# Optimization experiments

Hardware: AMD Instinct MI355X
Metric: run time of the kernel (lower is better)

Reference implementation:

```python
import jax, jax.numpy as jnp
import numpy as np
from jax.scipy.special import i0

# torchkbnufft default configuration
N = 256          # image size per dim (im_size)
OSF = 2          # grid oversampling factor (default grid_size = 2*im_size)
G = N * OSF      # oversampled grid size = 512
W = 6            # kernel width (numpoints default)
ALPHA = 2.34 * W # Kaiser-Bessel shape parameter (kbwidth default 2.34)
M = 65536        # number of non-uniform k-space samples
B, C = 2, 8      # batch, coils


def _kb_ft(t):
    """Analytic Fourier transform of the KB kernel (for deapodization)."""
    s2 = ALPHA ** 2 - (jnp.pi * W * t) ** 2
    z = jnp.sqrt(jnp.abs(s2)) + 1e-12
    return jnp.where(s2 >= 0, jnp.sinh(z) / z, jnp.sin(z) / z)


def _kb(d):
    """Kaiser-Bessel interpolation kernel, d = distance in grid units."""
    u = 1.0 - (2.0 * d / W) ** 2
    return jnp.where(u > 0, i0(ALPHA * jnp.sqrt(jnp.maximum(u, 1e-12))), 0.0) / W


def setup_inputs() -> dict:
    key = jax.random.key(0)
    k1, k2 = jax.random.split(key)
    x_image = jax.random.normal(k1, (B, C, N, N), dtype=jnp.float32)
    # trajectory in radians/sample, uniform in [-pi, pi)
    k_traj = (jax.random.uniform(k2, (2, M), dtype=jnp.float32) - 0.5) * (2 * jnp.pi)
    return {"x_image": x_image, "k_traj": k_traj}


def reference(x_image, k_traj):
    # 1) deapodization (scaling coefficients), centered image convention
    n = jnp.arange(N, dtype=jnp.float32) - N / 2
    sc = 1.0 / _kb_ft(n / G)                       # (N,)
    xs = (x_image * (sc[:, None] * sc[None, :])).astype(jnp.complex64)

    # 2) zero-pad onto oversampled grid with image centered at index 0 (mod G)
    grid = jnp.zeros(x_image.shape[:2] + (G, G), jnp.complex64)
    grid = grid.at[..., :N, :N].set(xs)
    grid = jnp.roll(grid, shift=(-(N // 2), -(N // 2)), axis=(-2, -1))
    Xk = jnp.fft.fft2(grid)                        # (B,C,G,G) uniform k-space

    # 3) KB interpolation onto non-uniform points (irregular gather)
    tm = k_traj * (G / (2 * jnp.pi))               # continuous grid coords, (2,M)
    offs = jnp.arange(-(W // 2) + 1, W // 2 + 1, dtype=jnp.float32)  # [-2..3]
    base = jnp.floor(tm)
    pts = base[:, :, None] + offs                  # (2,M,W) neighbor coords
    wts = _kb(tm[:, :, None] - pts)                # (2,M,W) real weights
    idx = pts.astype(jnp.int32) % G                # wrap (periodic grid)

    gathered = Xk[:, :, idx[0][:, :, None], idx[1][:, None, :]]  # (B,C,M,W,W)
    y = jnp.einsum('bcmij,mi,mj->bcm', gathered,
                   wts[0].astype(jnp.complex64), wts[1].astype(jnp.complex64))
    # return complex result as stacked (real, imag) float32 for the harness
    return jnp.stack([y.real, y.imag], axis=-1)   # (B,C,M,2)
```

## Files before the change

kernel.cpp:

```cpp
#include <hip/hip_runtime.h>
#include <hip/hip_fp16.h>
#include <math.h>

#define NN 256
#define GSZ 512
#define GG (GSZ * GSZ)
#define BC 16
#define MM 65536
#define ALPHA_C 14.04f
#define WKER 6
#define PI_F 3.14159265358979f
#define RC2 0.70710678118654752f
#define KSCALE 81.48733086305042f

#define SSCALE 16777216.0f
#define INV_SSCALE 5.9604644775390625e-8f

#define CAP 160
#define TRW 21
#define TPITCH 23
#define PLANE (TRW * TPITCH)
#define NPT16 (BC * TRW * TRW)

__device__ __forceinline__ __half2* gh_plane(float2* grid, int bc) {
    return (__half2*)((char*)grid + (size_t)bc * (GG * 8) + 524288);
}
__device__ __forceinline__ const __half2* gh_plane_c(const float2* grid, int bc) {
    return (const __half2*)((const char*)grid + (size_t)bc * (GG * 8) + 524288);
}


__device__ __forceinline__ float bessel_i0(float x) {
    if (x < 3.75f) {
        float t = x * (1.0f / 3.75f);
        float t2 = t * t;
        return 1.0f + t2 * (3.5156229f + t2 * (3.0899424f + t2 * (1.2067492f +
                     t2 * (0.2659732f + t2 * (0.0360768f + t2 * 0.0045813f)))));
    } else {
        float t = 3.75f / x;
        float p = 0.39894228f + t * (0.01328592f + t * (0.00225319f + t * (-0.00157565f +
                  t * (0.00916281f + t * (-0.02057706f + t * (0.02635537f +
                  t * (-0.01647633f + t * 0.00392377f)))))));
        return p * __expf(x) * rsqrtf(x);
    }
}

__device__ __forceinline__ float kb_weight(float d) {
    float r = d * (2.0f / (float)WKER);
    float u = 1.0f - r * r;
    if (u <= 0.0f) return 0.0f;
    return bessel_i0(ALPHA_C * sqrtf(u)) * (1.0f / (float)WKER);
}

__device__ __forceinline__ float kb_ft_inv(float t) {
    float a = PI_F * (float)WKER * t;
    float s2 = ALPHA_C * ALPHA_C - a * a;
    float z = sqrtf(fabsf(s2)) + 1e-12f;
    float sh = 0.5f * (__expf(z) - __expf(-z));
    return z / sh;
}

__device__ __forceinline__ void cmul(float& zr, float& zi, float wr, float wi) {
    float r = zr * wr - zi * wi;
    zi = zr * wi + zi * wr;
    zr = r;
}


template <int L>
__device__ __forceinline__ void radix8_stage(float* pr, float* pi_, int j) {
    int pos = j & (L - 1);
    int base = (j - pos) * 8 + pos;
    float ar[8], ai[8];
#pragma unroll
    for (int r = 0; r < 8; ++r) {
        int idx = base + r * L;
        int ph = idx + (idx >> 3);
        ar[r] = pr[ph];
        ai[r] = pi_[ph];
    }
    if (L > 1) {
        float th = (float)pos * (-PI_F / (4.0f * (float)L));
        float s1, c1;
        __sincosf(th, &s1, &c1);
        float wr = c1, wi = s1;
#pragma unroll
        for (int r = 1; r < 8; ++r) {
            cmul(ar[r], ai[r], wr, wi);
            float nr = wr * c1 - wi * s1;
            wi = wr * s1 + wi * c1;
            wr = nr;
        }
    }
    float s0r = ar[0] + ar[4], s0i = ai[0] + ai[4];
    float d0r = ar[0] - ar[4], d0i = ai[0] - ai[4];
    float s1r = ar[2] + ar[6], s1i = ai[2] + ai[6];
    float d1r = ar[2] - ar[6], d1i = ai[2] - ai[6];
    float E0r = s0r + s1r, E0i = s0i + s1i;
    float E2r = s0r - s1r, E2i = s0i - s1i;
    float E1r = d0r + d1i, E1i = d0i - d1r;
    float E3r = d0r - d1i, E3i = d0i + d1r;
    float u0r = ar[1] + ar[5], u0i = ai[1] + ai[5];
    float v0r = ar[1] - ar[5], v0i = ai[1] - ai[5];
    float u1r = ar[3] + ar[7], u1i = ai[3] + ai[7];
    float v1r = ar[3] - ar[7], v1i = ai[3] - ai[7];
    float O0r = u0r + u1r, O0i = u0i + u1i;
    float O2r = u0r - u1r, O2i = u0i - u1i;
    float O1r = v0r + v1i, O1i = v0i - v1r;
    float O3r = v0r - v1i, O3i = v0i + v1r;
    float t1r = RC2 * (O1r + O1i), t1i = RC2 * (O1i - O1r);
    float t2r = O2i,               t2i = -O2r;
    float t3r = RC2 * (O3i - O3r), t3i = -RC2 * (O3r + O3i);
    float xr[8], xi[8];
    xr[0] = E0r + O0r; xi[0] = E0i + O0i;
    xr[4] = E0r - O0r; xi[4] = E0i - O0i;
    xr[1] = E1r + t1r; xi[1] = E1i + t1i;
    xr[5] = E1r - t1r; xi[5] = E1i - t1i;
    xr[2] = E2r + t2r; xi[2] = E2i + t2i;
    xr[6] = E2r - t2r; xi[6] = E2i - t2i;
    xr[3] = E3r + t3r; xi[3] = E3i + t3i;
    xr[7] = E3r - t3r; xi[7] = E3i - t3i;
#pragma unroll
    for (int q = 0; q < 8; ++q) {
        int idx = base + q * L;
        int ph = idx + (idx >> 3);
        pr[ph] = xr[q];
        pi_[ph] = xi[q];
    }
}


#define LDSP 576
__global__ void __launch_bounds__(256) k_fft_row(const float* __restrict__ x,
                                                 float2* __restrict__ grid) {
    __shared__ float re[4][LDSP], im[4][LDSP];
    int b = blockIdx.x;
    int t = threadIdx.x;
    int w = t >> 6;
    int l = t & 63;
    int rg = (b & 63) * 4 + w;
    int bc = b >> 6;
    int r = (rg < 128) ? rg : rg + 256;
    int r_img = rg ^ 128;
    float scx = kb_ft_inv((float)(r_img - 128) * (1.0f / (float)GSZ));
    const float* xrow = x + ((size_t)bc * NN + (size_t)r_img) * NN;
#pragma unroll
    for (int e = 0; e < 8; ++e) {
        int i = e * 64 + l;
        float v = 0.0f;
        if (i < 128 || i >= 384) {
            int y = (i + 128) & (GSZ - 1);
            float scy = kb_ft_inv((float)(y - 128) * (1.0f / (float)GSZ));
            v = xrow[y] * scx * scy;
        }
        int rev = (l & 7) * 64 + (l >> 3) * 8 + e;
        int ph = rev + (rev >> 3);
        re[w][ph] = v;
        im[w][ph] = 0.0f;
    }
    __syncthreads();
    radix8_stage<1>(re[w], im[w], l);
    __syncthreads();
    radix8_stage<8>(re[w], im[w], l);
    __syncthreads();
    radix8_stage<64>(re[w], im[w], l);
    __syncthreads();
    size_t gbase = (size_t)bc * GG + (size_t)r * GSZ;
#pragma unroll
    for (int e = 0; e < 8; ++e) {
        int k = e * 64 + l;
        int ph = k + (k >> 3);
        grid[gbase + k] = make_float2(re[w][ph], im[w][ph]);
    }
}

#define CSTR 577
__global__ void __launch_bounds__(256) k_fft_col(float2* __restrict__ grid) {
    __shared__ float re[16][CSTR], im[16][CSTR];
    int b = blockIdx.x;
    int bc = b >> 5;
    int c0 = (b & 31) << 4;
    size_t base = (size_t)bc * GG + (size_t)c0;
    int t = threadIdx.x;
#pragma unroll
    for (int it = 0; it < 32; ++it) {
        int idx = it * 256 + t;
        int row = idx >> 4, col = idx & 15;
        float2 v = make_float2(0.0f, 0.0f);
        if (row < 128 || row >= 384)
            v = grid[base + (size_t)row * GSZ + col];
        int rev = (row & 7) * 64 + ((row >> 3) & 7) * 8 + (row >> 6);
        int ph = rev + (rev >> 3);
        re[col][ph] = v.x;
        im[col][ph] = v.y;
    }
    __syncthreads();
    int col = t & 15, jg = t >> 4;
#pragma unroll
    for (int k = 0; k < 4; ++k) radix8_stage<1>(re[col], im[col], jg + 16 * k);
    __syncthreads();
#pragma unroll
    for (int k = 0; k < 4; ++k) radix8_stage<8>(re[col], im[col], jg + 16 * k);
    __syncthreads();
#pragma unroll
    for (int k = 0; k < 4; ++k) radix8_stage<64>(re[col], im[col], jg + 16 * k);
    __syncthreads();
    __half2* ghp = gh_plane(grid, bc);
#pragma unroll
    for (int it = 0; it < 32; ++it) {
        int idx = it * 256 + t;
        int row = idx >> 4, c = idx & 15;
        int ph = row + (row >> 3);
        ghp[(size_t)row * GSZ + c0 + c] = __float22half2_rn(
            make_float2(re[c][ph] * SSCALE, im[c][ph] * SSCALE));
    }
}


__global__ void k_bin(const float* __restrict__ kt, unsigned* __restrict__ cnt,
                      unsigned short* __restrict__ ubuf) {
    int m = blockIdx.x * blockDim.x + threadIdx.x;
    float tmx = kt[m] * KSCALE;
    float tmy = kt[MM + m] * KSCALE;
    int ibx = (int)floorf(tmx) & (GSZ - 1);
    int iby = (int)floorf(tmy) & (GSZ - 1);
    int tile = ((ibx >> 4) << 5) | (iby >> 4);
    unsigned slot = atomicAdd(&cnt[tile], 1u);
    if (slot < CAP) ubuf[(size_t)tile * CAP + slot] = (unsigned short)m;
}


__device__ __forceinline__ void load_tile(const float2* __restrict__ grid, int tile,
                                          int t, __half2* buf) {
    int tx0 = (tile >> 5) << 4;
    int ty0 = (tile & 31) << 4;
#pragma unroll
    for (int k = 0; k < 28; ++k) {
        int idx = t + (k << 8);
        if (idx < NPT16) {
            int bcp = idx / (TRW * TRW);
            int rem = idx - bcp * (TRW * TRW);
            int r = rem / TRW;
            int c = rem - r * TRW;
            int row = (tx0 - 2 + r) & (GSZ - 1);
            int col = (ty0 - 2 + c) & (GSZ - 1);
            buf[k] = gh_plane_c(grid, bcp)[(size_t)row * GSZ + col];
        }
    }
}

__global__ void __launch_bounds__(256) k_gather_tile(
    const float2* __restrict__ grid, const float* __restrict__ kt,
    const unsigned* __restrict__ cnt, const unsigned short* __restrict__ ubuf,
    float2* __restrict__ out) {
    __shared__ __half2 ldsh[BC * PLANE];
    __shared__ float wts[CAP][13];
    __shared__ unsigned lxy[CAP];
    int bid = blockIdx.x;
    int b = ((bid & 7) << 6) | (bid >> 3);
    int t = threadIdx.x;
    __half2 buf[28];
    load_tile(grid, 2 * b, t, buf);
    for (int k2 = 0; k2 < 2; ++k2) {
        int tile = 2 * b + k2;
        int n = (int)cnt[tile];
        if (n > CAP) n = CAP;
        __syncthreads();
#pragma unroll
        for (int k = 0; k < 28; ++k) {
            int idx = t + (k << 8);
            if (idx < NPT16) {
                int bcp = idx / (TRW * TRW);
                int rem = idx - bcp * (TRW * TRW);
                int r = rem / TRW;
                int c = rem - r * TRW;
                ldsh[bcp * PLANE + r * TPITCH + c] = buf[k];
            }
        }
        if (t < n) {
            int m = (int)ubuf[(size_t)tile * CAP + t];
            float tmx = kt[m] * KSCALE;
            float tmy = kt[MM + m] * KSCALE;
            float bx = floorf(tmx), by = floorf(tmy);
#pragma unroll
            for (int o = 0; o < 6; ++o) {
                float offv = (float)(o - 2);
                wts[t][o]     = kb_weight(tmx - (bx + offv)) * INV_SSCALE;
                wts[t][6 + o] = kb_weight(tmy - (by + offv));
            }
            int lx = (int)bx & 15;
            int ly = (int)by & 15;
            lxy[t] = ((unsigned)m << 8) | (unsigned)(lx << 4) | (unsigned)ly;
        }
        __syncthreads();
        if (k2 == 0) load_tile(grid, 2 * b + 1, t, buf);
        int g = t >> 6;
        int base0 = (4 * g) * PLANE;
        for (int s = (t & 63); s < n; s += 64) {
            unsigned lc = lxy[s];
            int m = (int)(lc >> 8);
            int lx = (int)((lc >> 4) & 15u);
            int ly = (int)(lc & 15u);
            float w0v[6], w1v[6];
#pragma unroll
            for (int o = 0; o < 6; ++o) {
                w0v[o] = wts[s][o];
                w1v[o] = wts[s][6 + o];
            }
            int off0 = base0 + lx * TPITCH + ly;
            float ar[4] = {0.f, 0.f, 0.f, 0.f};
            float ai[4] = {0.f, 0.f, 0.f, 0.f};
#pragma unroll
            for (int ii = 0; ii < 6; ++ii) {
                float wi = w0v[ii];
                int rowoff = off0 + ii * TPITCH;
#pragma unroll
                for (int j = 0; j < 6; ++j) {
                    float wv = wi * w1v[j];
                    int o = rowoff + j;
#pragma unroll
                    for (int bq = 0; bq < 4; ++bq) {
                        float2 v = __half22float2(ldsh[o + bq * PLANE]);
                        ar[bq] = fmaf(wv, v.x, ar[bq]);
                        ai[bq] = fmaf(wv, v.y, ai[bq]);
                    }
                }
            }
#pragma unroll
            for (int bq = 0; bq < 4; ++bq)
                out[(size_t)(4 * g + bq) * MM + m] = make_float2(ar[bq], ai[bq]);
        }
    }
}

__global__ void k_gather(const float2* __restrict__ grid, const float* __restrict__ kt,
                         float2* __restrict__ out) {
    int tid = blockIdx.x * blockDim.x + threadIdx.x;
    int m = tid & (MM - 1);
    int bc = tid >> 16;
    float tmx = kt[m] * KSCALE;
    float tmy = kt[MM + m] * KSCALE;
    float bx = floorf(tmx), by = floorf(tmy);
    int ibx = (int)bx, iby = (int)by;
    float w0[6], w1[6];
    int ix[6], iy[6];
#pragma unroll
    for (int o = 0; o < 6; ++o) {
        float offv = (float)(o - 2);
        w0[o] = kb_weight(tmx - (bx + offv)) * INV_SSCALE;
        w1[o] = kb_weight(tmy - (by + offv));
        ix[o] = (ibx + (o - 2) + GSZ) & (GSZ - 1);
        iy[o] = (iby + (o - 2) + GSZ) & (GSZ - 1);
    }
    const __half2* img = gh_plane_c(grid, bc);
    float ar = 0.0f, ai = 0.0f;
#pragma unroll
    for (int i = 0; i < 6; ++i) {
        const __half2* rowp = img + (size_t)ix[i] * GSZ;
        float wi = w0[i];
#pragma unroll
        for (int j = 0; j < 6; ++j) {
            float2 v = __half22float2(rowp[iy[j]]);
            float wv = wi * w1[j];
            ar = fmaf(wv, v.x, ar);
            ai = fmaf(wv, v.y, ai);
        }
    }
    out[(size_t)bc * MM + m] = make_float2(ar, ai);
}


extern "C" void kernel_launch(void* const* d_in, const int* in_sizes, int n_in,
                              void* d_out, int out_size, void* d_ws, size_t ws_size,
                              hipStream_t stream) {
    const float* x = (const float*)d_in[0];
    const float* kt = (const float*)d_in[1];
    float2* out = (float2*)d_out;
    char* ws = (char*)d_ws;

    const size_t GRID_BYTES = (size_t)BC * GG * sizeof(float2);
    const size_t CNT_BYTES = 1024 * sizeof(unsigned);
    const size_t UBUF_BYTES = (size_t)1024 * CAP * sizeof(unsigned short);
    float2* grid = (float2*)ws;
    unsigned* cnt = (unsigned*)(ws + GRID_BYTES);
    unsigned short* ubuf = (unsigned short*)(ws + GRID_BYTES + CNT_BYTES);
    const size_t NEED = GRID_BYTES + CNT_BYTES + UBUF_BYTES;

    if (ws_size >= NEED) {
        hipMemsetAsync(cnt, 0, CNT_BYTES, stream);
        k_bin<<<MM / 256, 256, 0, stream>>>(kt, cnt, ubuf);
        k_fft_row<<<BC * 64, 256, 0, stream>>>(x, grid);
        k_fft_col<<<BC * (GSZ / 16), 256, 0, stream>>>(grid);
        k_gather_tile<<<512, 256, 0, stream>>>(grid, kt, cnt, ubuf, out);
    } else {
        k_fft_row<<<BC * 64, 256, 0, stream>>>(x, grid);
        k_fft_col<<<BC * (GSZ / 16), 256, 0, stream>>>(grid);
        k_gather<<<(BC * MM) / 256, 256, 0, stream>>>(grid, kt, out);
    }
}
```

Baseline: 76.07 us.

## Split gather tile work across coil quads with smaller blocks

After: 77.50 us. Within noise of the previous version (+1.9%).

```diff
diff --git a/kernel.cpp b/kernel.cpp
--- a/kernel.cpp
+++ b/kernel.cpp
@@ -20,7 +20,8 @@
 #define TRW 21
 #define TPITCH 23
 #define PLANE (TRW * TPITCH)
-#define NPT16 (BC * TRW * TRW)
+#define QPL 4
+#define NPQ (QPL * TRW * TRW)
 
 __device__ __forceinline__ __half2* gh_plane(float2* grid, int bc) {
     return (__half2*)((char*)grid + (size_t)bc * (GG * 8) + 524288);
@@ -230,106 +231,88 @@
 }
 
 
-__device__ __forceinline__ void load_tile(const float2* __restrict__ grid, int tile,
-                                          int t, __half2* buf) {
+__global__ void __launch_bounds__(128) k_gather_tile(
+    const float2* __restrict__ grid, const float* __restrict__ kt,
+    const unsigned* __restrict__ cnt, const unsigned short* __restrict__ ubuf,
+    float2* __restrict__ out) {
+    __shared__ __half2 ldsh[QPL * PLANE];
+    __shared__ float wts[CAP][13];
+    __shared__ unsigned lxy[CAP];
+    int bid = blockIdx.x;
+    int b = ((bid & 7) << 9) | (bid >> 3);
+    int tile = b >> 2;
+    int quad = b & 3;
+    int bc0 = quad * QPL;
     int tx0 = (tile >> 5) << 4;
     int ty0 = (tile & 31) << 4;
-#pragma unroll
-    for (int k = 0; k < 28; ++k) {
-        int idx = t + (k << 8);
-        if (idx < NPT16) {
-            int bcp = idx / (TRW * TRW);
-            int rem = idx - bcp * (TRW * TRW);
+    int t = threadIdx.x;
+#pragma unroll
+    for (int k = 0; k < 14; ++k) {
+        int idx = t + (k << 7);
+        if (idx < NPQ) {
+            int p = idx / (TRW * TRW);
+            int rem = idx - p * (TRW * TRW);
             int r = rem / TRW;
             int c = rem - r * TRW;
             int row = (tx0 - 2 + r) & (GSZ - 1);
             int col = (ty0 - 2 + c) & (GSZ - 1);
-            buf[k] = gh_plane_c(grid, bcp)[(size_t)row * GSZ + col];
-        }
-    }
-}
-
-__global__ void __launch_bounds__(256) k_gather_tile(
-    const float2* __restrict__ grid, const float* __restrict__ kt,
-    const unsigned* __restrict__ cnt, const unsigned short* __restrict__ ubuf,
-    float2* __restrict__ out) {
-    __shared__ __half2 ldsh[BC * PLANE];
-    __shared__ float wts[CAP][13];
-    __shared__ unsigned lxy[CAP];
-    int bid = blockIdx.x;
-    int b = ((bid & 7) << 6) | (bid >> 3);
-    int t = threadIdx.x;
-    __half2 buf[28];
-    load_tile(grid, 2 * b, t, buf);
-    for (int k2 = 0; k2 < 2; ++k2) {
-        int tile = 2 * b + k2;
-        int n = (int)cnt[tile];
-        if (n > CAP) n = CAP;
-        __syncthreads();
-#pragma unroll
-        for (int k = 0; k < 28; ++k) {
-            int idx = t + (k << 8);
-            if (idx < NPT16) {
-                int bcp = idx / (TRW * TRW);
-                int rem = idx - bcp * (TRW * TRW);
-                int r = rem / TRW;
-                int c = rem - r * TRW;
-                ldsh[bcp * PLANE + r * TPITCH + c] = buf[k];
+            ldsh[p * PLANE + r * TPITCH + c] =
+                gh_plane_c(grid, bc0 + p)[(size_t)row * GSZ + col];
+        }
+    }
+    int n = (int)cnt[tile];
+    if (n > CAP) n = CAP;
+    for (int p = t; p < n; p += 128) {
+        int m = (int)ubuf[(size_t)tile * CAP + p];
+        float tmx = kt[m] * KSCALE;
+        float tmy = kt[MM + m] * KSCALE;
+        float bx = floorf(tmx), by = floorf(tmy);
+#pragma unroll
+        for (int o = 0; o < 6; ++o) {
+            float offv = (float)(o - 2);
+            wts[p][o]     = kb_weight(tmx - (bx + offv)) * INV_SSCALE;
+            wts[p][6 + o] = kb_weight(tmy - (by + offv));
+        }
+        int lx = (int)bx & 15;
+        int ly = (int)by & 15;
+        lxy[p] = ((unsigned)m << 8) | (unsigned)(lx << 4) | (unsigned)ly;
+    }
+    __syncthreads();
+    int g = t >> 6;
+    int baseA = (2 * g) * PLANE;
+    int baseB = baseA + PLANE;
+    int bcA = bc0 + 2 * g, bcB = bcA + 1;
+    for (int s = (t & 63); s < n; s += 64) {
+        unsigned lc = lxy[s];
+        int m = (int)(lc >> 8);
+        int lx = (int)((lc >> 4) & 15u);
+        int ly = (int)(lc & 15u);
+        float w0v[6], w1v[6];
+#pragma unroll
+        for (int o = 0; o < 6; ++o) {
+            w0v[o] = wts[s][o];
+            w1v[o] = wts[s][6 + o];
+        }
+        int off0 = lx * TPITCH + ly;
+        float arA = 0.f, aiA = 0.f, arB = 0.f, aiB = 0.f;
+#pragma unroll
+        for (int ii = 0; ii < 6; ++ii) {
+            float wi = w0v[ii];
+            int rowoff = off0 + ii * TPITCH;
+#pragma unroll
+            for (int j = 0; j < 6; ++j) {
+                float wv = wi * w1v[j];
+                int o = rowoff + j;
+                float2 vA = __half22float2(ldsh[baseA + o]);
+                float2 vB = __half22float2(ldsh[baseB + o]);
+                arA = fmaf(wv, vA.x, arA);
+                aiA = fmaf(wv, vA.y, aiA);
+                arB = fmaf(wv, vB.x, arB);
+                aiB = fmaf(wv, vB.y, aiB);
             }
         }
-        if (t < n) {
-            int m = (int)ubuf[(size_t)tile * CAP + t];
-            float tmx = kt[m] * KSCALE;
-            float tmy = kt[MM + m] * KSCALE;
-            float bx = floorf(tmx), by = floorf(tmy);
-#pragma unroll
-            for (int o = 0; o < 6; ++o) {
-                float offv = (float)(o - 2);
-                wts[t][o]     = kb_weight(tmx - (bx + offv)) * INV_SSCALE;
-                wts[t][6 + o] = kb_weight(tmy - (by + offv));
-            }
-            int lx = (int)bx & 15;
-            int ly = (int)by & 15;
-            lxy[t] = ((unsigned)m << 8) | (unsigned)(lx << 4) | (unsigned)ly;
-        }
-        __syncthreads();
-        if (k2 == 0) load_tile(grid, 2 * b + 1, t, buf);
-        int g = t >> 6;
-        int base0 = (4 * g) * PLANE;
-        for (int s = (t & 63); s < n; s += 64) {
-            unsigned lc = lxy[s];
-            int m = (int)(lc >> 8);
-            int lx = (int)((lc >> 4) & 15u);
-            int ly = (int)(lc & 15u);
-            float w0v[6], w1v[6];
-#pragma unroll
-            for (int o = 0; o < 6; ++o) {
-                w0v[o] = wts[s][o];
-                w1v[o] = wts[s][6 + o];
-            }
-            int off0 = base0 + lx * TPITCH + ly;
-            float ar[4] = {0.f, 0.f, 0.f, 0.f};
-            float ai[4] = {0.f, 0.f, 0.f, 0.f};
-#pragma unroll
-            for (int ii = 0; ii < 6; ++ii) {
-                float wi = w0v[ii];
-                int rowoff = off0 + ii * TPITCH;
-#pragma unroll
-                for (int j = 0; j < 6; ++j) {
-                    float wv = wi * w1v[j];
-                    int o = rowoff + j;
-#pragma unroll
-                    for (int bq = 0; bq < 4; ++bq) {
-                        float2 v = __half22float2(ldsh[o + bq * PLANE]);
-                        ar[bq] = fmaf(wv, v.x, ar[bq]);
-                        ai[bq] = fmaf(wv, v.y, ai[bq]);
-                    }
-                }
-            }
-#pragma unroll
-            for (int bq = 0; bq < 4; ++bq)
-                out[(size_t)(4 * g + bq) * MM + m] = make_float2(ar[bq], ai[bq]);
-        }
+        out[(size_t)bcA * MM + m] = make_float2(arA, aiA);
+        out[(size_t)bcB * MM + m] = make_float2(arB, aiB);
     }
 }
 
@@ -391,7 +374,7 @@
         k_bin<<<MM / 256, 256, 0, stream>>>(kt, cnt, ubuf);
         k_fft_row<<<BC * 64, 256, 0, stream>>>(x, grid);
         k_fft_col<<<BC * (GSZ / 16), 256, 0, stream>>>(grid);
-        k_gather_tile<<<512, 256, 0, stream>>>(grid, kt, cnt, ubuf, out);
+        k_gather_tile<<<4096, 128, 0, stream>>>(grid, kt, cnt, ubuf, out);
     } else {
         k_fft_row<<<BC * 64, 256, 0, stream>>>(x, grid);
         k_fft_col<<<BC * (GSZ / 16), 256, 0, stream>>>(grid);
```
